# Kernel optimization log

Measured on AMD Instinct MI355X. Metric: run time of the kernel, lower is better.

Reference implementation:

```python
import jax, jax.numpy as jnp
import numpy as np

EMB = 1024
HEADS = 16

def setup_inputs() -> dict:
    key = jax.random.key(0)
    ks = jax.random.split(key, 5)
    s = 1.0 / np.sqrt(EMB)
    x = jax.random.normal(ks[0], (2, 2048, EMB), dtype=jnp.float32)
    W_qkv = jax.random.normal(ks[1], (EMB, 3 * EMB), dtype=jnp.float32) * s
    b_qkv = jnp.zeros((3 * EMB,), dtype=jnp.float32)
    W_out = jax.random.normal(ks[2], (EMB, EMB), dtype=jnp.float32) * s
    b_out = jnp.zeros((EMB,), dtype=jnp.float32)
    return {"x": x, "W_qkv": W_qkv, "b_qkv": b_qkv, "W_out": W_out, "b_out": b_out}

def reference(x, W_qkv, b_qkv, W_out, b_out):
    B, N, C = x.shape
    H = HEADS
    D = C // H
    qkv = x @ W_qkv + b_qkv                      # [B,N,3C]
    qkv = qkv.reshape(B, N, 3, H, D)
    q, k, v = (qkv[:, :, i].transpose(0, 2, 1, 3) for i in range(3))  # [B,H,N,D]
    # NOTE: original scales by C**-0.5 (full embed dim), not head dim
    scale = C ** (-0.5)
    attn = jnp.einsum('bhnd,bhmd->bhnm', q, k) * scale
    attn = jax.nn.softmax(attn, axis=-1)
    out = jnp.einsum('bhnm,bhmd->bhnd', attn, v)  # [B,H,N,D]
    out = out.transpose(0, 2, 1, 3).reshape(B, N, C)
    return out @ W_out + b_out
```

## Files before the change

### kernel.cpp

```cpp
#include <hip/hip_runtime.h>
#include <hip/hip_bf16.h>
#include <cstdint>
#include <cstddef>

typedef __bf16 bf16;
typedef __bf16 bf16x4 __attribute__((ext_vector_type(4)));
typedef __bf16 bf16x8 __attribute__((ext_vector_type(8)));
typedef float f32x4 __attribute__((ext_vector_type(4)));

#define LOG2E 1.4426950408889634f
#define QSCALE (0.03125f * LOG2E)
#define PSHIFT 8.0f

#define GLD16(gp, lp)                                                              \
  __builtin_amdgcn_global_load_lds((__attribute__((address_space(1))) void*)(gp),  \
                                   (__attribute__((address_space(3))) void*)(lp),  \
                                   16, 0, 0)

__global__ void k_prep(const float* __restrict__ x, const float* __restrict__ Wqkv,
                       const float* __restrict__ Wout, bf16* __restrict__ xb,
                       bf16* __restrict__ wqT, bf16* __restrict__ woT) {
  const int blk = blockIdx.x, tid = threadIdx.x;
  if (blk < 2048) {
    int i = (blk * 256 + tid) * 8;
    const float4* p = (const float4*)(x + i);
    float4 a = p[0], b = p[1];
    bf16x8 o;
    o[0] = (bf16)a.x; o[1] = (bf16)a.y; o[2] = (bf16)a.z; o[3] = (bf16)a.w;
    o[4] = (bf16)b.x; o[5] = (bf16)b.y; o[6] = (bf16)b.z; o[7] = (bf16)b.w;
    *(bf16x8*)(xb + i) = o;
    return;
  }
  const float* in;
  bf16* out;
  int R = 1024, C, bx, by;
  if (blk < 2048 + 3072) {
    in = Wqkv; out = wqT; C = 3072;
    bx = (blk - 2048) % 96; by = (blk - 2048) / 96;
  } else {
    in = Wout; out = woT; C = 1024;
    bx = (blk - 5120) % 32; by = (blk - 5120) / 32;
  }
  __shared__ float t[32][33];
  const int tx = tid & 31, ty = tid >> 5;
  int c0 = bx * 32, r0 = by * 32;
#pragma unroll
  for (int i = 0; i < 4; i++)
    t[ty + i * 8][tx] = in[(size_t)(r0 + ty + i * 8) * C + c0 + tx];
  __syncthreads();
#pragma unroll
  for (int i = 0; i < 4; i++)
    out[(size_t)(c0 + ty + i * 8) * R + r0 + tx] = (bf16)t[tx][ty + i * 8];
}

template <int EPI>
__global__ __launch_bounds__(256, 2) void k_gemm_bt(
    const bf16* __restrict__ A, const bf16* __restrict__ Bt,
    const float* __restrict__ bias, float* __restrict__ outF,
    bf16* __restrict__ qb, bf16* __restrict__ kb, bf16* __restrict__ vb) {
  __shared__ __align__(16) bf16 As[128 * 32];
  __shared__ __align__(16) bf16 Bs[128 * 32];
  const int tid = threadIdx.x;
  const int lane = tid & 63, w = tid >> 6;
  const int quad = lane >> 4, l16 = lane & 15;
  const int wm = (w >> 1) * 64, wn = (w & 1) * 64;
  const int bm = blockIdx.y * 128, bn = blockIdx.x * 128;
  f32x4 acc[4][4] = {};

  for (int kt = 0; kt < 1024; kt += 32) {
    __syncthreads();
#pragma unroll
    for (int p = 0; p < 2; p++) {
      int idx = p * 256 + tid;
      int row = idx >> 2, bq = idx & 3;
      int gb = (bq - ((row >> 1) & 3)) & 3;
      GLD16(A + (size_t)(bm + row) * 1024 + kt + gb * 8, As + idx * 8);
      GLD16(Bt + (size_t)(bn + row) * 1024 + kt + gb * 8, Bs + idx * 8);
    }
    __syncthreads();

    bf16x8 af[4], bfr[4];
#pragma unroll
    for (int mi = 0; mi < 4; mi++) {
      int row = wm + mi * 16 + l16;
      int bq = (quad + ((row >> 1) & 3)) & 3;
      af[mi] = *(const bf16x8*)(As + row * 32 + bq * 8);
    }
#pragma unroll
    for (int ni = 0; ni < 4; ni++) {
      int row = wn + ni * 16 + l16;
      int bq = (quad + ((row >> 1) & 3)) & 3;
      bfr[ni] = *(const bf16x8*)(Bs + row * 32 + bq * 8);
    }
#pragma unroll
    for (int mi = 0; mi < 4; mi++)
#pragma unroll
      for (int ni = 0; ni < 4; ni++)
        acc[mi][ni] =
            __builtin_amdgcn_mfma_f32_16x16x32_bf16(af[mi], bfr[ni], acc[mi][ni], 0, 0, 0);
  }

#pragma unroll
  for (int ni = 0; ni < 4; ni++) {
    int col = bn + wn + ni * 16 + l16;
    float bv = bias[col];
    if (EPI == 1) {
#pragma unroll
      for (int mi = 0; mi < 4; mi++)
#pragma unroll
        for (int r = 0; r < 4; r++) {
          int row = bm + wm + mi * 16 + quad * 4 + r;
          outF[(size_t)row * 1024 + col] = acc[mi][ni][r] + bv;
        }
    } else {
      int which = col >> 10, cc = col & 1023;
      int h = cc >> 6, d = cc & 63;
      if (which == 2) {
#pragma unroll
        for (int mi = 0; mi < 4; mi++) {
          int rowb = bm + wm + mi * 16 + quad * 4;
          int b = rowb >> 11, n0 = rowb & 2047;
          bf16x4 vv;
#pragma unroll
          for (int r = 0; r < 4; r++) vv[r] = (bf16)(acc[mi][ni][r] + bv);
          *(bf16x4*)(vb + ((size_t)(b * 16 + h) * 64 + d) * 2048 + n0) = vv;
        }
      } else {
#pragma unroll
        for (int mi = 0; mi < 4; mi++)
#pragma unroll
          for (int r = 0; r < 4; r++) {
            int row = bm + wm + mi * 16 + quad * 4 + r;
            int b = row >> 11, n = row & 2047;
            float v = acc[mi][ni][r] + bv;
            if (which == 0)
              qb[((size_t)(b * 16 + h) * 2048 + n) * 64 + d] = (bf16)(v * QSCALE);
            else
              kb[((size_t)(b * 16 + h) * 2048 + n) * 64 + d] = (bf16)v;
          }
      }
    }
  }
}

__global__ __launch_bounds__(256, 4) void k_flash(
    const bf16* __restrict__ Q, const bf16* __restrict__ K,
    const bf16* __restrict__ V, bf16* __restrict__ O) {
  __shared__ __align__(16) bf16 Kt[2][64 * 64];
  __shared__ __align__(16) bf16 Vt[2][64 * 64];
  __shared__ __align__(16) bf16 Pb[4][16 * 64];
  const int tid = threadIdx.x;
  const int lane = tid & 63, w = tid >> 6;
  const int quad = lane >> 4, l16 = lane & 15;
  const int bh = blockIdx.y, qt = blockIdx.x;
  const bf16* qh = Q + (size_t)bh * 2048 * 64;
  const bf16* kh = K + (size_t)bh * 2048 * 64;
  const bf16* vh = V + (size_t)bh * 64 * 2048;

  bf16x8 qf[2];
#pragma unroll
  for (int kc = 0; kc < 2; kc++)
    qf[kc] = *(const bf16x8*)(qh + (size_t)(qt * 64 + w * 16 + l16) * 64 + kc * 32 + quad * 8);

  bf16x8 ones;
#pragma unroll
  for (int j = 0; j < 8; j++) ones[j] = (bf16)1.0f;

  f32x4 o[4] = {};
  f32x4 lacc = {};

  bf16* pw = &Pb[w][0];

  auto stage = [&](int kt2, int buf) {
#pragma unroll
    for (int p = 0; p < 2; p++) {
      int idx = p * 256 + tid;
      int row = idx >> 3, bq = idx & 7, gb = bq ^ (row & 7);
      GLD16(kh + (size_t)(kt2 * 64 + row) * 64 + gb * 8, &Kt[buf][idx * 8]);
      GLD16(vh + (size_t)row * 2048 + kt2 * 64 + gb * 8, &Vt[buf][idx * 8]);
    }
  };

  stage(0, 0);

  for (int kt2 = 0; kt2 < 32; kt2++) {
    const int p = kt2 & 1;
    __syncthreads();
    if (kt2 < 31) stage(kt2 + 1, p ^ 1);
    const bf16* Kb = &Kt[p][0];
    const bf16* Vb = &Vt[p][0];

    f32x4 s[4];
#pragma unroll
    for (int nj = 0; nj < 4; nj++) {
      int row = nj * 16 + l16;
      bf16x8 kf0 = *(const bf16x8*)(Kb + row * 64 + ((quad ^ (row & 7)) << 3));
      bf16x8 kf1 = *(const bf16x8*)(Kb + row * 64 + (((4 + quad) ^ (row & 7)) << 3));
      f32x4 t = {-PSHIFT, -PSHIFT, -PSHIFT, -PSHIFT};
      t = __builtin_amdgcn_mfma_f32_16x16x32_bf16(kf0, qf[0], t, 0, 0, 0);
      t = __builtin_amdgcn_mfma_f32_16x16x32_bf16(kf1, qf[1], t, 0, 0, 0);
      s[nj] = t;
    }

    {
      bf16* pr = pw + l16 * 64;
#pragma unroll
      for (int nj = 0; nj < 4; nj++) {
        bf16x4 pk;
#pragma unroll
        for (int r = 0; r < 4; r++) pk[r] = (bf16)__builtin_amdgcn_exp2f(s[nj][r]);
        int blk = (nj * 2 + (quad >> 1)) ^ (l16 & 7);
        *(bf16x4*)(pr + blk * 8 + (quad & 1) * 4) = pk;
      }
    }

#pragma unroll
    for (int kc = 0; kc < 2; kc++) {
      bf16x8 pf =
          *(const bf16x8*)(pw + l16 * 64 + (((kc * 4 + quad) ^ (l16 & 7)) << 3));
      lacc = __builtin_amdgcn_mfma_f32_16x16x32_bf16(ones, pf, lacc, 0, 0, 0);
#pragma unroll
      for (int nd = 0; nd < 4; nd++) {
        int row = nd * 16 + l16;
        bf16x8 vf = *(const bf16x8*)(Vb + row * 64 + (((kc * 4 + quad) ^ (row & 7)) << 3));
        o[nd] = __builtin_amdgcn_mfma_f32_16x16x32_bf16(vf, pf, o[nd], 0, 0, 0);
      }
    }
  }

  const int b = bh >> 4, h = bh & 15;
  float inv = 1.0f / lacc[0];
  int n = qt * 64 + w * 16 + l16;
#pragma unroll
  for (int nd = 0; nd < 4; nd++) {
    bf16x4 ov;
#pragma unroll
    for (int r = 0; r < 4; r++) ov[r] = (bf16)(o[nd][r] * inv);
    int c = h * 64 + nd * 16 + quad * 4;
    *(bf16x4*)(O + ((size_t)b * 2048 + n) * 1024 + c) = ov;
  }
}


extern "C" void kernel_launch(void* const* d_in, const int* in_sizes, int n_in,
                              void* d_out, int out_size, void* d_ws, size_t ws_size,
                              hipStream_t stream) {
  (void)in_sizes; (void)n_in; (void)out_size; (void)ws_size;
  const float* x    = (const float*)d_in[0];
  const float* Wqkv = (const float*)d_in[1];
  const float* bqkv = (const float*)d_in[2];
  const float* Wout = (const float*)d_in[3];
  const float* bout = (const float*)d_in[4];
  float* out = (float*)d_out;

  char* ws = (char*)d_ws;
  size_t off = 0;
  auto take = [&](size_t bytes) {
    char* p = ws + off;
    off += (bytes + 255) & ~(size_t)255;
    return p;
  };
  bf16* xb   = (bf16*)take((size_t)4096 * 1024 * 2);
  bf16* wqT  = (bf16*)take((size_t)3072 * 1024 * 2);
  bf16* woT  = (bf16*)take((size_t)1024 * 1024 * 2);
  bf16* qbuf = (bf16*)take((size_t)32 * 2048 * 64 * 2);
  bf16* kbuf = (bf16*)take((size_t)32 * 2048 * 64 * 2);
  bf16* vbuf = (bf16*)take((size_t)32 * 2048 * 64 * 2);
  bf16* aout = (bf16*)take((size_t)4096 * 1024 * 2);

  k_prep<<<6144, 256, 0, stream>>>(x, Wqkv, Wout, xb, wqT, woT);
  k_gemm_bt<0><<<dim3(24, 32), 256, 0, stream>>>(xb, wqT, bqkv, nullptr, qbuf, kbuf, vbuf);
  k_flash<<<dim3(32, 32), 256, 0, stream>>>(qbuf, kbuf, vbuf, aout);
  k_gemm_bt<1><<<dim3(8, 32), 256, 0, stream>>>(aout, woT, bout, out, nullptr, nullptr, nullptr);
}
```

Measured before the change: 189.1 us.

## Rewrite flash attention with 32x32 MFMA and register-resident probabilities

The attention kernel now uses 32x32x16 bf16 MFMAs, with each wave covering 32 query rows, so each block handles 128 query rows. The exponentiated scores are packed straight from the accumulator registers into B-operand fragments, which removes the LDS round trip through the P buffer. The row sum is accumulated in scalar registers instead of with an extra MFMA against a ones vector. The grid is flattened to 512 blocks with a swizzled block-to-tile map, and launch bounds drop to 2 blocks per CU. The costs are higher register use, fewer blocks, and half-width V fragment loads.

```diff
diff --git a/kernel.cpp b/kernel.cpp
--- a/kernel.cpp
+++ b/kernel.cpp
@@ -7,6 +7,7 @@
 typedef __bf16 bf16x4 __attribute__((ext_vector_type(4)));
 typedef __bf16 bf16x8 __attribute__((ext_vector_type(8)));
 typedef float f32x4 __attribute__((ext_vector_type(4)));
+typedef float f32x16 __attribute__((ext_vector_type(16)));
 
 #define LOG2E 1.4426950408889634f
 #define QSCALE (0.03125f * LOG2E)
@@ -143,38 +144,34 @@
   }
 }
 
-__global__ __launch_bounds__(256, 4) void k_flash(
+__global__ __launch_bounds__(256, 2) void k_flash(
     const bf16* __restrict__ Q, const bf16* __restrict__ K,
     const bf16* __restrict__ V, bf16* __restrict__ O) {
   __shared__ __align__(16) bf16 Kt[2][64 * 64];
   __shared__ __align__(16) bf16 Vt[2][64 * 64];
-  __shared__ __align__(16) bf16 Pb[4][16 * 64];
   const int tid = threadIdx.x;
   const int lane = tid & 63, w = tid >> 6;
-  const int quad = lane >> 4, l16 = lane & 15;
-  const int bh = blockIdx.y, qt = blockIdx.x;
+  const int l31 = lane & 31, h = lane >> 5;
+  const int x7 = l31 & 7;
+  const int cid = ((blockIdx.x & 7) << 6) | (blockIdx.x >> 3);
+  const int qt = cid & 15, bh = cid >> 4;
   const bf16* qh = Q + (size_t)bh * 2048 * 64;
   const bf16* kh = K + (size_t)bh * 2048 * 64;
   const bf16* vh = V + (size_t)bh * 64 * 2048;
-
-  bf16x8 qf[2];
-#pragma unroll
-  for (int kc = 0; kc < 2; kc++)
-    qf[kc] = *(const bf16x8*)(qh + (size_t)(qt * 64 + w * 16 + l16) * 64 + kc * 32 + quad * 8);
-
-  bf16x8 ones;
-#pragma unroll
-  for (int j = 0; j < 8; j++) ones[j] = (bf16)1.0f;
-
-  f32x4 o[4] = {};
-  f32x4 lacc = {};
-
-  bf16* pw = &Pb[w][0];
+  const int qrow = qt * 128 + w * 32 + l31;
+
+  bf16x8 qf[4];
+#pragma unroll
+  for (int c4 = 0; c4 < 4; c4++)
+    qf[c4] = *(const bf16x8*)(qh + (size_t)qrow * 64 + c4 * 16 + h * 8);
+
+  f32x16 o0 = {}, o1 = {};
+  float ls0 = 0.f, ls1 = 0.f, ls2 = 0.f, ls3 = 0.f;
 
   auto stage = [&](int kt2, int buf) {
 #pragma unroll
-    for (int p = 0; p < 2; p++) {
-      int idx = p * 256 + tid;
+    for (int pp = 0; pp < 2; pp++) {
+      int idx = pp * 256 + tid;
       int row = idx >> 3, bq = idx & 7, gb = bq ^ (row & 7);
       GLD16(kh + (size_t)(kt2 * 64 + row) * 64 + gb * 8, &Kt[buf][idx * 8]);
       GLD16(vh + (size_t)row * 2048 + kt2 * 64 + gb * 8, &Vt[buf][idx * 8]);
@@ -190,54 +187,68 @@
     const bf16* Kb = &Kt[p][0];
     const bf16* Vb = &Vt[p][0];
 
-    f32x4 s[4];
-#pragma unroll
-    for (int nj = 0; nj < 4; nj++) {
-      int row = nj * 16 + l16;
-      bf16x8 kf0 = *(const bf16x8*)(Kb + row * 64 + ((quad ^ (row & 7)) << 3));
-      bf16x8 kf1 = *(const bf16x8*)(Kb + row * 64 + (((4 + quad) ^ (row & 7)) << 3));
-      f32x4 t = {-PSHIFT, -PSHIFT, -PSHIFT, -PSHIFT};
-      t = __builtin_amdgcn_mfma_f32_16x16x32_bf16(kf0, qf[0], t, 0, 0, 0);
-      t = __builtin_amdgcn_mfma_f32_16x16x32_bf16(kf1, qf[1], t, 0, 0, 0);
-      s[nj] = t;
-    }
-
+    f32x16 a0, a1;
+#pragma unroll
+    for (int j = 0; j < 16; j++) { a0[j] = -PSHIFT; a1[j] = -PSHIFT; }
     {
-      bf16* pr = pw + l16 * 64;
-#pragma unroll
-      for (int nj = 0; nj < 4; nj++) {
-        bf16x4 pk;
-#pragma unroll
-        for (int r = 0; r < 4; r++) pk[r] = (bf16)__builtin_amdgcn_exp2f(s[nj][r]);
-        int blk = (nj * 2 + (quad >> 1)) ^ (l16 & 7);
-        *(bf16x4*)(pr + blk * 8 + (quad & 1) * 4) = pk;
+      const bf16* k0 = Kb + l31 * 64;
+      const bf16* k1 = Kb + (32 + l31) * 64;
+#pragma unroll
+      for (int c4 = 0; c4 < 4; c4++) {
+        int off = ((2 * c4 + h) ^ x7) << 3;
+        bf16x8 kf0 = *(const bf16x8*)(k0 + off);
+        bf16x8 kf1 = *(const bf16x8*)(k1 + off);
+        a0 = __builtin_amdgcn_mfma_f32_32x32x16_bf16(kf0, qf[c4], a0, 0, 0, 0);
+        a1 = __builtin_amdgcn_mfma_f32_32x32x16_bf16(kf1, qf[c4], a1, 0, 0, 0);
       }
     }
 
-#pragma unroll
-    for (int kc = 0; kc < 2; kc++) {
-      bf16x8 pf =
-          *(const bf16x8*)(pw + l16 * 64 + (((kc * 4 + quad) ^ (l16 & 7)) << 3));
-      lacc = __builtin_amdgcn_mfma_f32_16x16x32_bf16(ones, pf, lacc, 0, 0, 0);
-#pragma unroll
-      for (int nd = 0; nd < 4; nd++) {
-        int row = nd * 16 + l16;
-        bf16x8 vf = *(const bf16x8*)(Vb + row * 64 + (((kc * 4 + quad) ^ (row & 7)) << 3));
-        o[nd] = __builtin_amdgcn_mfma_f32_16x16x32_bf16(vf, pf, o[nd], 0, 0, 0);
+    bf16x8 pf[4];
+#pragma unroll
+    for (int j = 0; j < 16; j++) {
+      float e0 = __builtin_amdgcn_exp2f(a0[j]);
+      float e1 = __builtin_amdgcn_exp2f(a1[j]);
+      bf16 p0 = (bf16)e0, p1 = (bf16)e1;
+      pf[j >> 3][j & 7] = p0;
+      pf[2 + (j >> 3)][j & 7] = p1;
+      if (j & 1) { ls1 += (float)p0; ls3 += (float)p1; }
+      else       { ls0 += (float)p0; ls2 += (float)p1; }
+    }
+
+    {
+      const bf16* v0 = Vb + l31 * 64 + 4 * h;
+      const bf16* v1 = Vb + (32 + l31) * 64 + 4 * h;
+#pragma unroll
+      for (int c4 = 0; c4 < 4; c4++) {
+        int b0i = (c4 >> 1) * 4 + (c4 & 1) * 2;
+        int e0 = ((b0i ^ x7) << 3), e1 = (((b0i + 1) ^ x7) << 3);
+        bf16x8 vf0 = __builtin_shufflevector(*(const bf16x4*)(v0 + e0),
+                                             *(const bf16x4*)(v0 + e1),
+                                             0, 1, 2, 3, 4, 5, 6, 7);
+        bf16x8 vf1 = __builtin_shufflevector(*(const bf16x4*)(v1 + e0),
+                                             *(const bf16x4*)(v1 + e1),
+                                             0, 1, 2, 3, 4, 5, 6, 7);
+        o0 = __builtin_amdgcn_mfma_f32_32x32x16_bf16(vf0, pf[c4], o0, 0, 0, 0);
+        o1 = __builtin_amdgcn_mfma_f32_32x32x16_bf16(vf1, pf[c4], o1, 0, 0, 0);
       }
     }
   }
 
-  const int b = bh >> 4, h = bh & 15;
-  float inv = 1.0f / lacc[0];
-  int n = qt * 64 + w * 16 + l16;
-#pragma unroll
-  for (int nd = 0; nd < 4; nd++) {
-    bf16x4 ov;
-#pragma unroll
-    for (int r = 0; r < 4; r++) ov[r] = (bf16)(o[nd][r] * inv);
-    int c = h * 64 + nd * 16 + quad * 4;
-    *(bf16x4*)(O + ((size_t)b * 2048 + n) * 1024 + c) = ov;
+  float lsum = (ls0 + ls1) + (ls2 + ls3);
+  lsum += __shfl_xor(lsum, 32, 64);
+  float inv = 1.0f / lsum;
+  const int bb = bh >> 4, hh = bh & 15;
+  bf16* orow = O + ((size_t)bb * 2048 + qrow) * 1024 + hh * 64;
+#pragma unroll
+  for (int g = 0; g < 4; g++) {
+    bf16x4 ov0, ov1;
+#pragma unroll
+    for (int r = 0; r < 4; r++) {
+      ov0[r] = (bf16)(o0[4 * g + r] * inv);
+      ov1[r] = (bf16)(o1[4 * g + r] * inv);
+    }
+    *(bf16x4*)(orow + 8 * g + 4 * h) = ov0;
+    *(bf16x4*)(orow + 32 + 8 * g + 4 * h) = ov1;
   }
 }
 
@@ -270,6 +281,6 @@
 
   k_prep<<<6144, 256, 0, stream>>>(x, Wqkv, Wout, xb, wqT, woT);
   k_gemm_bt<0><<<dim3(24, 32), 256, 0, stream>>>(xb, wqT, bqkv, nullptr, qbuf, kbuf, vbuf);
-  k_flash<<<dim3(32, 32), 256, 0, stream>>>(qbuf, kbuf, vbuf, aout);
+  k_flash<<<dim3(512), 256, 0, stream>>>(qbuf, kbuf, vbuf, aout);
   k_gemm_bt<1><<<dim3(8, 32), 256, 0, stream>>>(aout, woT, bout, out, nullptr, nullptr, nullptr);
 }
```

New measurement: 187.6 us. About the same (-0.8%).
